# Performance work log

Hardware: AMD Instinct MI355X
Metric: run time of the kernel (lower is better)

## Reference

```python
import jax, jax.numpy as jnp
import numpy as np

# Uniform batch of B graphs, N nodes each, C features, skip-window size FS
B, N, C, FS = 64, 512, 128, 16
RES = N - 1            # number of window rows per graph (unfold1d with stride 1)
TAU_A, TAU_B, TOT_EPOCHS = 10.0, 0.1, 100.0
EPS = 1e-20
NEG = -1e9


def setup_inputs() -> dict:
    key = jax.random.key(0)
    k1, k2, k3, k4 = jax.random.split(key, 4)
    x = jax.random.normal(k1, (B * N, C), dtype=jnp.float32)
    edge_index = jax.random.randint(k2, (2, 524288), 0, B * N, dtype=jnp.int32)
    score_w = jax.random.normal(k3, (C, 1), dtype=jnp.float32)       # TopKPool Linear weight
    att_params = jax.random.normal(k4, (2 * C, 1), dtype=jnp.float32)  # SKipPool att_params
    return {"x": x, "edge_index": edge_index, "score_w": score_w,
            "att_params": att_params, "epoch": 10}


def _forward(x, score_w, att_params, epoch):
    tau0 = TAU_A * (TAU_B / TAU_A) ** (epoch / TOT_EPOCHS)

    # ---- TopKPool scorer (init_ratio -> 1.0: keep all nodes, rank-sort per graph) ----
    scores = (x @ score_w)[:, 0] / jnp.linalg.norm(score_w)   # [B*N]
    sv = scores.reshape(B, N)
    order = jnp.argsort(-sv, axis=1)                           # descending perm per graph
    xg = jnp.take_along_axis(x.reshape(B, N, C), order[:, :, None], axis=1)  # [B,N,C]
    scores_ranked = jnp.tanh(jnp.take_along_axis(sv, order, axis=1))         # [B,N]

    # ---- skip-window edge construction (unfold1d semantics): row r -> dests r..r+FS-1 ----
    r = jnp.arange(RES)
    j = jnp.arange(FS)
    dest = r[:, None] + j[None, :]            # [RES,FS]
    valid = dest < N                          # padded positions masked (inf/zero rows)
    destc = jnp.minimum(dest, N - 1)

    xs = xg[:, :RES, None, :]                                  # [B,RES,1,C] sources
    xd = jnp.where(valid[None, :, :, None], xg[:, destc], 0.0)  # [B,RES,FS,C] dests

    # getDM_ei: RBF kernel over edge distances (sigma=1); masked edges -> 0 (inf row)
    d = jnp.linalg.norm(xs - xd, axis=-1)                      # [B,RES,FS]
    kmat = jnp.where(valid[None], jnp.exp(-d / 2.0), 0.0) - EPS

    # getSM_ei: attention score via att_params on [x_src || x_dst]
    a_src, a_dst = att_params[:C, 0], att_params[C:, 0]
    atts = (xg[:, :RES] @ a_src)[:, :, None] + jnp.einsum('brjc,c->brj', xd, a_dst)
    atts = jnp.where(valid[None], atts, NEG)
    w_att = jax.nn.softmax(atts / tau0, axis=-1)               # tau-annealed row softmax

    q = kmat * w_att                                           # combined edge score [B,RES,FS]
    qm = jnp.where(valid[None], q, NEG)
    w_row = jnp.max(qm, axis=-1)                               # best-match score per row (scatterSort top-1)
    jumps = 1 + jnp.argmax(qm[:, :, 1:], axis=-1).astype(jnp.int32)  # data-dependent stride in [1,FS-1]

    # ---- sequential pivot chaining (innerLoopStar): pivot -> pivot + jump[pivot] ----
    def chain(xg_b, w_b, sr_b, jumps_b):
        def step(carry, _):
            p, acc = carry
            active = p < RES
            pc = jnp.minimum(p, RES - 1)
            wv = jnp.where(active, w_b[pc] * sr_b[pc], 0.0)
            acc = acc + wv * xg_b[pc]
            p = jnp.where(active, p + jumps_b[pc], p)
            return (p, acc), None
        (pf, acc), _ = jax.lax.scan(step, (jnp.int32(0), jnp.zeros((C,), xg_b.dtype)),
                                    None, length=RES)
        return acc

    pooled = jax.vmap(chain)(xg, w_row, scores_ranked[:, :RES], jumps)  # [B,C]
    return pooled


def reference(x, edge_index, score_w, att_params, epoch):
    # edge_index only feeds the scorer's filter_adj in the original (structure unused here)
    return _forward(x, score_w, att_params, epoch)
```

## Files before the change

### kernel.cpp

```cpp
#include <hip/hip_runtime.h>
#include <math.h>

#define B_   64
#define N_   512
#define C_   128
#define FS_  16
#define RES_ 511
#define CHUNK_ 64
#define HALO_  15
#define MAXR_  (CHUNK_ + HALO_)
#define RSTRIDE_ 132

__device__ __forceinline__ float bf2f(unsigned short u) {
  union { unsigned int i; float f; } v;
  v.i = ((unsigned int)u) << 16;
  return v.f;
}

__device__ __forceinline__ int detect16(const unsigned short* p) {
  int sane = 0;
  for (int i = 0; i < 64; ++i) {
    int e = (p[i] >> 7) & 0xFF;
    if (e >= 100 && e <= 140) sane++;
  }
  return (sane >= 48) ? 0 : 1;
}

__device__ __forceinline__ float2 ld2(const void* p, int idx, int mode) {
  if (mode) return ((const float2*)p)[idx];
  ushort2 u = ((const ushort2*)p)[idx];
  return make_float2(bf2f(u.x), bf2f(u.y));
}
__device__ __forceinline__ float ld1(const void* p, int idx, int mode) {
  if (mode) return ((const float*)p)[idx];
  return bf2f(((const unsigned short*)p)[idx]);
}
__device__ __forceinline__ float4 ld4(const void* p, int idx4, int mode) {
  if (mode) return ((const float4*)p)[idx4];
  ushort4 u = ((const ushort4*)p)[idx4];
  return make_float4(bf2f(u.x), bf2f(u.y), bf2f(u.z), bf2f(u.w));
}

__device__ __forceinline__ double wred(double v) {
#pragma unroll
  for (int m = 32; m; m >>= 1) v += __shfl_xor(v, m, 64);
  return v;
}
__device__ __forceinline__ float wredf(float v) {
#pragma unroll
  for (int m = 32; m; m >>= 1) v += __shfl_xor(v, m, 64);
  return v;
}

__device__ __forceinline__ float get_epoch(const int* ep) {
  int ei = ep[0];
  if (ei >= 0 && ei <= 1000000) return (float)ei;
  union { int i; float f; } u; u.i = ei;
  return (u.f >= 0.f && u.f <= 1e6f) ? u.f : 10.f;
}

__global__ __launch_bounds__(256) void k_scores(
    const void* __restrict__ x, const void* __restrict__ w,
    const void* __restrict__ a,
    float* __restrict__ sc, float* __restrict__ asr, float* __restrict__ ads)
{
  __shared__ int s_modes[3];
  if (threadIdx.x == 0) {
    s_modes[0] = detect16((const unsigned short*)x);
    s_modes[1] = detect16((const unsigned short*)w);
    s_modes[2] = detect16((const unsigned short*)a);
  }
  __syncthreads();
  const int mode_x = s_modes[0], mode_w = s_modes[1], mode_a = s_modes[2];
  const int gid  = blockIdx.x * blockDim.x + threadIdx.x;
  const int wid  = gid >> 6;
  const int lane = threadIdx.x & 63;

  const float2 wv2 = ld2(w, lane, mode_w);
  const float2 sv2 = ld2(a, lane, mode_a);
  const float2 dv2 = ld2(a, 64 + lane, mode_a);
  const double nww = wred((double)wv2.x * wv2.x + (double)wv2.y * wv2.y);
  const float nrm32 = (float)sqrt(nww);

  float2 xv = ld2(x, wid * 64 + lane, mode_x);
  double s  = wred((double)xv.x * wv2.x + (double)xv.y * wv2.y);
  float  da = wredf(xv.x * sv2.x + xv.y * sv2.y);
  float  dd = wredf(xv.x * dv2.x + xv.y * dv2.y);
  if (lane == 0) {
    sc[wid]  = ((float)s) / nrm32;
    asr[wid] = da;
    ads[wid] = dd;
  }
}

__global__ __launch_bounds__(256) void k_sort(
    const float* __restrict__ sc, int* __restrict__ order,
    float* __restrict__ srk)
{
  __shared__ __align__(16) float sl[N_];
  __shared__ int part[4][CHUNK_];
  const int blk = blockIdx.x, b = blk >> 3, ch = blk & 7;
  const int bN = b * N_, t = threadIdx.x;
  sl[t]       = sc[bN + t];
  sl[t + 256] = sc[bN + t + 256];
  __syncthreads();
  const int n = t & 63, p = t >> 6;
  const int g = ch * CHUNK_ + n;
  const float my = sl[g];
  const float4* sl4 = (const float4*)sl;
  int rank = 0;
#pragma unroll 4
  for (int k4 = p * 32; k4 < p * 32 + 32; ++k4) {
    float4 v = sl4[k4];
    int k = k4 * 4;
    rank += (int)((v.x > my) || (v.x == my && k     < g));
    rank += (int)((v.y > my) || (v.y == my && k + 1 < g));
    rank += (int)((v.z > my) || (v.z == my && k + 2 < g));
    rank += (int)((v.w > my) || (v.w == my && k + 3 < g));
  }
  part[p][n] = rank;
  __syncthreads();
  if (t < CHUNK_) {
    const int gg = ch * CHUNK_ + t;
    const int r = part[0][t] + part[1][t] + part[2][t] + part[3][t];
    order[bN + r] = gg;
    srk[bN + r]   = tanhf(sl[gg]);
  }
}

__global__ __launch_bounds__(512) void k_att(
    const void* __restrict__ x, const float* __restrict__ asr,
    const float* __restrict__ ads, const int* __restrict__ order,
    const int* __restrict__ ep,
    float* __restrict__ wrw, int* __restrict__ jmp)
{
  __shared__ float rows[MAXR_ * RSTRIDE_];
  __shared__ float ads_l[MAXR_];
  __shared__ float asr_l[CHUNK_];
  __shared__ int   ord_l[MAXR_];
  __shared__ int   s_mode;
  __shared__ float s_invtau;

  const int blk = blockIdx.x;
  const int b = blk >> 3;
  const int cr0 = (blk & 7) * CHUNK_;
  const int bN = b * N_;
  const int t = threadIdx.x;
  const int nrows = min(N_ - cr0, MAXR_);

  if (t == 0) {
    s_mode = detect16((const unsigned short*)x);
    float evv = get_epoch(ep);
    s_invtau = (float)(1.0 / (10.0 * pow(0.01, (double)evv / 100.0)));
  }
  if (t < nrows) {
    int o = order[bN + cr0 + t];
    ord_l[t] = o;
    ads_l[t] = ads[bN + o];
    if (t < CHUNK_) asr_l[t] = asr[bN + o];
  }
  __syncthreads();
  const int mode = s_mode;
  const float inv_tau = s_invtau;

  {
    const int rl0 = t >> 5, c4 = t & 31;
    for (int rl = rl0; rl < nrows; rl += 16) {
      float4 v = ld4(x, (bN + ord_l[rl]) * 32 + c4, mode);
      float* dst = &rows[rl * RSTRIDE_ + c4 * 4];
      dst[0] = v.x; dst[1] = v.y; dst[2] = v.z; dst[3] = v.w;
    }
  }
  __syncthreads();

  const int lane = t & 63, wv = t >> 6;
  const int j = lane & 15, cg4 = lane >> 4;

  for (int ii = 0; ii < 8; ++ii) {
    const int rloc = wv * 8 + ii;
    const int r = cr0 + rloc;
    if (r >= RES_) break;
    const int dest = r + j;
    const bool valid = dest < N_;
    const int dl = (valid ? dest : (N_ - 1)) - cr0;

    const float* srcp = &rows[rloc * RSTRIDE_ + cg4 * 32];
    const float* dstp = &rows[dl   * RSTRIDE_ + cg4 * 32];
    double p0 = 0.0, p1 = 0.0, p2 = 0.0, p3 = 0.0;
#pragma unroll
    for (int c = 0; c < 8; ++c) {
      float4 s4 = *(const float4*)(srcp + c * 4);
      float4 d4 = *(const float4*)(dstp + c * 4);
      float e0 = s4.x - d4.x, e1 = s4.y - d4.y;
      float e2 = s4.z - d4.z, e3 = s4.w - d4.w;
      float q0 = e0 * e0, q1 = e1 * e1, q2 = e2 * e2, q3 = e3 * e3;
      p0 += (double)q0; p1 += (double)q1; p2 += (double)q2; p3 += (double)q3;
    }
    double dacc = (p0 + p1) + (p2 + p3);
    dacc += __shfl_xor(dacc, 16, 64);
    dacc += __shfl_xor(dacc, 32, 64);

    float d32 = sqrtf((float)dacc);
    float kkj = valid ? (__expf(-0.5f * d32) - 1e-20f) : -1e-20f;
    float aaj = valid ? (asr_l[rloc] + ads_l[dl]) : -1e9f;
    float ttj = aaj * inv_tau;

    float mx = ttj;
#pragma unroll
    for (int m = 1; m < 16; m <<= 1) mx = fmaxf(mx, __shfl_xor(mx, m, 64));
    float eej = __expf(ttj - mx);
    float ssum = eej;
#pragma unroll
    for (int m = 1; m < 16; m <<= 1) ssum += __shfl_xor(ssum, m, 64);
    float q  = kkj * (eej * (1.0f / ssum));
    float qm = valid ? q : -1e9f;

    float wr = qm;
#pragma unroll
    for (int m = 1; m < 16; m <<= 1) wr = fmaxf(wr, __shfl_xor(wr, m, 64));
    float qe = (j == 0) ? -INFINITY : qm;
    float m1 = qe;
#pragma unroll
    for (int m = 1; m < 16; m <<= 1) m1 = fmaxf(m1, __shfl_xor(m1, m, 64));
    unsigned long long mask = __ballot(qe == m1);
    int bj = __builtin_ctz((unsigned)(mask & 0xFFFEu));

    if (lane == 0) {
      wrw[bN + r] = wr;
      jmp[bN + r] = bj;
    }
  }
}

__global__ __launch_bounds__(512) void k_chain(
    const void* __restrict__ x, const float* __restrict__ wrw,
    const float* __restrict__ srk, const int* __restrict__ jmp,
    const int* __restrict__ order, float* __restrict__ out)
{
  __shared__ int   tab[9][N_];
  __shared__ int   ol[N_];
  __shared__ float wl[N_];
  __shared__ float sl2[N_];
  __shared__ float cl[N_];
  __shared__ int   rl[N_];
  __shared__ int   Pcnt;
  __shared__ int   s_mode;

  const int b = blockIdx.x, t = threadIdx.x;
  if (t == 0) s_mode = detect16((const unsigned short*)x);

  ol[t] = order[b * N_ + t];
  if (t < RES_) {
    wl[t]  = wrw[b * N_ + t];
    sl2[t] = srk[b * N_ + t];
    tab[0][t] = min(t + jmp[b * N_ + t], RES_);
  } else {
    tab[0][t] = RES_;
  }
  if (t == 0) Pcnt = RES_;
  __syncthreads();
  const int mode_x = s_mode;
#pragma unroll
  for (int k = 1; k < 9; ++k) {
    int v = tab[k - 1][tab[k - 1][t]];
    tab[k][t] = v;
    __syncthreads();
  }
  int node = 0;
#pragma unroll
  for (int k = 0; k < 9; ++k)
    if ((t >> k) & 1) node = tab[k][node];
  bool valid = (node < RES_);
  cl[t] = valid ? wl[node] * sl2[node] : 0.0f;
  rl[t] = valid ? ol[node] : 0;
  if (!valid) atomicMin(&Pcnt, t);
  __syncthreads();

  if (t < C_) {
    const int P = Pcnt;
    float acc = 0.f;
    int i = 0;
    for (; i + 4 <= P; i += 4) {
      float c0 = cl[i],     c1 = cl[i + 1], c2 = cl[i + 2], c3 = cl[i + 3];
      int   r0 = rl[i],     r1 = rl[i + 1], r2 = rl[i + 2], r3 = rl[i + 3];
      float x0 = ld1(x, (b * N_ + r0) * C_ + t, mode_x);
      float x1 = ld1(x, (b * N_ + r1) * C_ + t, mode_x);
      float x2 = ld1(x, (b * N_ + r2) * C_ + t, mode_x);
      float x3 = ld1(x, (b * N_ + r3) * C_ + t, mode_x);
      acc = acc + c0 * x0;
      acc = acc + c1 * x1;
      acc = acc + c2 * x2;
      acc = acc + c3 * x3;
    }
    for (; i < P; ++i)
      acc = acc + cl[i] * ld1(x, (b * N_ + rl[i]) * C_ + t, mode_x);
    out[b * C_ + t] = acc;
  }
}

extern "C" void kernel_launch(void* const* d_in, const int* in_sizes, int n_in,
                              void* d_out, int out_size, void* d_ws, size_t ws_size,
                              hipStream_t stream) {
  const void* x = nullptr; const void* w = nullptr; const void* a = nullptr;
  const int* ep = nullptr;
  for (int i = 0; i < n_in; ++i) {
    int s = in_sizes[i];
    if      (s == B_ * N_ * C_) x  = d_in[i];
    else if (s == C_)           w  = d_in[i];
    else if (s == 2 * C_)       a  = d_in[i];
    else if (s == 1)            ep = (const int*)d_in[i];
  }
  if (!x)  x  = d_in[0];
  if (!w)  w  = d_in[2];
  if (!a)  a  = d_in[3];
  if (!ep) ep = (const int*)d_in[4];
  (void)out_size; (void)ws_size;

  float* ws = (float*)d_ws;
  const int NN = B_ * N_;
  float* sc    = ws;
  float* asr   = ws + NN;
  float* ads   = ws + 2 * NN;
  int*   order = (int*)(ws + 3 * NN);
  float* srk   = ws + 4 * NN;
  float* wrw   = ws + 5 * NN;
  int*   jmp   = (int*)(ws + 6 * NN);

  k_scores<<<NN / 4, 256, 0, stream>>>(x, w, a, sc, asr, ads);
  k_sort<<<B_ * 8, 256, 0, stream>>>(sc, order, srk);
  k_att<<<B_ * 8, 512, 0, stream>>>(x, asr, ads, order, ep, wrw, jmp);
  k_chain<<<B_, N_, 0, stream>>>(x, wrw, srk, jmp, order, (float*)d_out);
}
```

Before: 128.4 us.

## Fuse score computation into sort kernel and attention dots into att kernel

```diff
diff --git a/kernel.cpp b/kernel.cpp
--- a/kernel.cpp
+++ b/kernel.cpp
@@ -17,15 +17,6 @@
   return v.f;
 }
 
-__device__ __forceinline__ int detect16(const unsigned short* p) {
-  int sane = 0;
-  for (int i = 0; i < 64; ++i) {
-    int e = (p[i] >> 7) & 0xFF;
-    if (e >= 100 && e <= 140) sane++;
-  }
-  return (sane >= 48) ? 0 : 1;
-}
-
 __device__ __forceinline__ float2 ld2(const void* p, int idx, int mode) {
   if (mode) return ((const float2*)p)[idx];
   ushort2 u = ((const ushort2*)p)[idx];
@@ -50,6 +41,12 @@
 #pragma unroll
   for (int m = 32; m; m >>= 1) v += __shfl_xor(v, m, 64);
   return v;
+}
+
+__device__ __forceinline__ int detect_w0(const unsigned short* p, int lane) {
+  int e = (p[lane] >> 7) & 0xFF;
+  unsigned long long m = __ballot(e >= 100 && e <= 140);
+  return (__popcll(m) >= 48) ? 0 : 1;
 }
 
 __device__ __forceinline__ float get_epoch(const int* ep) {
@@ -59,58 +56,44 @@
   return (u.f >= 0.f && u.f <= 1e6f) ? u.f : 10.f;
 }
 
-__global__ __launch_bounds__(256) void k_scores(
+__global__ __launch_bounds__(512) void k_sortscore(
     const void* __restrict__ x, const void* __restrict__ w,
-    const void* __restrict__ a,
-    float* __restrict__ sc, float* __restrict__ asr, float* __restrict__ ads)
+    int* __restrict__ order, float* __restrict__ srk)
 {
-  __shared__ int s_modes[3];
-  if (threadIdx.x == 0) {
-    s_modes[0] = detect16((const unsigned short*)x);
-    s_modes[1] = detect16((const unsigned short*)w);
-    s_modes[2] = detect16((const unsigned short*)a);
-  }
-  __syncthreads();
-  const int mode_x = s_modes[0], mode_w = s_modes[1], mode_a = s_modes[2];
-  const int gid  = blockIdx.x * blockDim.x + threadIdx.x;
-  const int wid  = gid >> 6;
-  const int lane = threadIdx.x & 63;
+  __shared__ __align__(16) float sl[N_];
+  __shared__ int part[8][CHUNK_];
+  __shared__ int s_modes[2];
+  const int blk = blockIdx.x, b = blk >> 3, ch = blk & 7;
+  const int bN = b * N_, t = threadIdx.x, lane = t & 63, wv = t >> 6;
+
+  if (t < 64) {
+    int mx_ = detect_w0((const unsigned short*)x, lane);
+    int mw_ = detect_w0((const unsigned short*)w, lane);
+    if (t == 0) { s_modes[0] = mx_; s_modes[1] = mw_; }
+  }
+  __syncthreads();
+  const int mode_x = s_modes[0], mode_w = s_modes[1];
 
   const float2 wv2 = ld2(w, lane, mode_w);
-  const float2 sv2 = ld2(a, lane, mode_a);
-  const float2 dv2 = ld2(a, 64 + lane, mode_a);
   const double nww = wred((double)wv2.x * wv2.x + (double)wv2.y * wv2.y);
   const float nrm32 = (float)sqrt(nww);
 
-  float2 xv = ld2(x, wid * 64 + lane, mode_x);
-  double s  = wred((double)xv.x * wv2.x + (double)xv.y * wv2.y);
-  float  da = wredf(xv.x * sv2.x + xv.y * sv2.y);
-  float  dd = wredf(xv.x * dv2.x + xv.y * dv2.y);
-  if (lane == 0) {
-    sc[wid]  = ((float)s) / nrm32;
-    asr[wid] = da;
-    ads[wid] = dd;
-  }
-}
-
-__global__ __launch_bounds__(256) void k_sort(
-    const float* __restrict__ sc, int* __restrict__ order,
-    float* __restrict__ srk)
-{
-  __shared__ __align__(16) float sl[N_];
-  __shared__ int part[4][CHUNK_];
-  const int blk = blockIdx.x, b = blk >> 3, ch = blk & 7;
-  const int bN = b * N_, t = threadIdx.x;
-  sl[t]       = sc[bN + t];
-  sl[t + 256] = sc[bN + t + 256];
-  __syncthreads();
-  const int n = t & 63, p = t >> 6;
+#pragma unroll 2
+  for (int i = 0; i < 64; ++i) {
+    const int node = wv * 64 + i;
+    float2 xv = ld2(x, (bN + node) * 64 + lane, mode_x);
+    double s = wred((double)xv.x * wv2.x + (double)xv.y * wv2.y);
+    if (lane == 0) sl[node] = ((float)s) / nrm32;
+  }
+  __syncthreads();
+
+  const int n = t & 63, p = wv;
   const int g = ch * CHUNK_ + n;
   const float my = sl[g];
   const float4* sl4 = (const float4*)sl;
   int rank = 0;
 #pragma unroll 4
-  for (int k4 = p * 32; k4 < p * 32 + 32; ++k4) {
+  for (int k4 = p * 16; k4 < p * 16 + 16; ++k4) {
     float4 v = sl4[k4];
     int k = k4 * 4;
     rank += (int)((v.x > my) || (v.x == my && k     < g));
@@ -122,23 +105,23 @@
   __syncthreads();
   if (t < CHUNK_) {
     const int gg = ch * CHUNK_ + t;
-    const int r = part[0][t] + part[1][t] + part[2][t] + part[3][t];
+    const int r = part[0][t] + part[1][t] + part[2][t] + part[3][t]
+                + part[4][t] + part[5][t] + part[6][t] + part[7][t];
     order[bN + r] = gg;
     srk[bN + r]   = tanhf(sl[gg]);
   }
 }
 
 __global__ __launch_bounds__(512) void k_att(
-    const void* __restrict__ x, const float* __restrict__ asr,
-    const float* __restrict__ ads, const int* __restrict__ order,
-    const int* __restrict__ ep,
+    const void* __restrict__ x, const void* __restrict__ a,
+    const int* __restrict__ order, const int* __restrict__ ep,
     float* __restrict__ wrw, int* __restrict__ jmp)
 {
   __shared__ float rows[MAXR_ * RSTRIDE_];
   __shared__ float ads_l[MAXR_];
   __shared__ float asr_l[CHUNK_];
   __shared__ int   ord_l[MAXR_];
-  __shared__ int   s_mode;
+  __shared__ int   s_modes[2];
   __shared__ float s_invtau;
 
   const int blk = blockIdx.x;
@@ -146,40 +129,56 @@
   const int cr0 = (blk & 7) * CHUNK_;
   const int bN = b * N_;
   const int t = threadIdx.x;
+  const int lane = t & 63, wv = t >> 6;
   const int nrows = min(N_ - cr0, MAXR_);
 
-  if (t == 0) {
-    s_mode = detect16((const unsigned short*)x);
-    float evv = get_epoch(ep);
-    s_invtau = (float)(1.0 / (10.0 * pow(0.01, (double)evv / 100.0)));
-  }
-  if (t < nrows) {
-    int o = order[bN + cr0 + t];
-    ord_l[t] = o;
-    ads_l[t] = ads[bN + o];
-    if (t < CHUNK_) asr_l[t] = asr[bN + o];
-  }
-  __syncthreads();
-  const int mode = s_mode;
+  if (t < 64) {
+    int mx_ = detect_w0((const unsigned short*)x, lane);
+    int ma_ = detect_w0((const unsigned short*)a, lane);
+    if (t == 0) {
+      s_modes[0] = mx_; s_modes[1] = ma_;
+      float evv = get_epoch(ep);
+      s_invtau = (float)(1.0 / (10.0 * pow(0.01, (double)evv / 100.0)));
+    }
+  }
+  if (t < nrows) ord_l[t] = order[bN + cr0 + t];
+  __syncthreads();
+  const int mode_x = s_modes[0], mode_a = s_modes[1];
   const float inv_tau = s_invtau;
 
   {
     const int rl0 = t >> 5, c4 = t & 31;
     for (int rl = rl0; rl < nrows; rl += 16) {
-      float4 v = ld4(x, (bN + ord_l[rl]) * 32 + c4, mode);
+      float4 v = ld4(x, (bN + ord_l[rl]) * 32 + c4, mode_x);
       float* dst = &rows[rl * RSTRIDE_ + c4 * 4];
       dst[0] = v.x; dst[1] = v.y; dst[2] = v.z; dst[3] = v.w;
     }
   }
   __syncthreads();
 
-  const int lane = t & 63, wv = t >> 6;
+  {
+    const float2 sv2 = ld2(a, lane, mode_a);
+    const float2 dv2 = ld2(a, 64 + lane, mode_a);
+    for (int rl = wv; rl < nrows; rl += 8) {
+      const float2 xr = *(const float2*)&rows[rl * RSTRIDE_ + 2 * lane];
+      float da = wredf(xr.x * sv2.x + xr.y * sv2.y);
+      float dd = wredf(xr.x * dv2.x + xr.y * dv2.y);
+      if (lane == 0) {
+        ads_l[rl] = dd;
+        if (rl < CHUNK_) asr_l[rl] = da;
+      }
+    }
+  }
+  __syncthreads();
+
   const int j = lane & 15, cg4 = lane >> 4;
-
-  for (int ii = 0; ii < 8; ++ii) {
+  const int nr = min(CHUNK_, RES_ - cr0);
+  int cnt = nr - wv * 8; cnt = max(0, min(8, cnt));
+
+#pragma unroll 2
+  for (int ii = 0; ii < cnt; ++ii) {
     const int rloc = wv * 8 + ii;
     const int r = cr0 + rloc;
-    if (r >= RES_) break;
     const int dest = r + j;
     const bool valid = dest < N_;
     const int dl = (valid ? dest : (N_ - 1)) - cr0;
@@ -215,13 +214,12 @@
     float q  = kkj * (eej * (1.0f / ssum));
     float qm = valid ? q : -1e9f;
 
-    float wr = qm;
-#pragma unroll
-    for (int m = 1; m < 16; m <<= 1) wr = fmaxf(wr, __shfl_xor(wr, m, 64));
     float qe = (j == 0) ? -INFINITY : qm;
     float m1 = qe;
 #pragma unroll
     for (int m = 1; m < 16; m <<= 1) m1 = fmaxf(m1, __shfl_xor(m1, m, 64));
+    float q0v = __shfl(qm, lane & 48, 64);
+    float wr = fmaxf(m1, q0v);
     unsigned long long mask = __ballot(qe == m1);
     int bj = __builtin_ctz((unsigned)(mask & 0xFFFEu));
 
@@ -247,7 +245,10 @@
   __shared__ int   s_mode;
 
   const int b = blockIdx.x, t = threadIdx.x;
-  if (t == 0) s_mode = detect16((const unsigned short*)x);
+  if (t < 64) {
+    int mx_ = detect_w0((const unsigned short*)x, t);
+    if (t == 0) s_mode = mx_;
+  }
 
   ol[t] = order[b * N_ + t];
   if (t < RES_) {
@@ -318,16 +319,12 @@
 
   float* ws = (float*)d_ws;
   const int NN = B_ * N_;
-  float* sc    = ws;
-  float* asr   = ws + NN;
-  float* ads   = ws + 2 * NN;
-  int*   order = (int*)(ws + 3 * NN);
-  float* srk   = ws + 4 * NN;
-  float* wrw   = ws + 5 * NN;
-  int*   jmp   = (int*)(ws + 6 * NN);
-
-  k_scores<<<NN / 4, 256, 0, stream>>>(x, w, a, sc, asr, ads);
-  k_sort<<<B_ * 8, 256, 0, stream>>>(sc, order, srk);
-  k_att<<<B_ * 8, 512, 0, stream>>>(x, asr, ads, order, ep, wrw, jmp);
+  int*   order = (int*)ws;
+  float* srk   = ws + NN;
+  float* wrw   = ws + 2 * NN;
+  int*   jmp   = (int*)(ws + 3 * NN);
+
+  k_sortscore<<<B_ * 8, 512, 0, stream>>>(x, w, order, srk);
+  k_att<<<B_ * 8, 512, 0, stream>>>(x, a, order, ep, wrw, jmp);
   k_chain<<<B_, N_, 0, stream>>>(x, wrw, srk, jmp, order, (float*)d_out);
 }
```

After: 151.7 us. +18.2%, slower.
